# Performance work log

Hardware: AMD Instinct MI355X
Metric: run time of the kernel (lower is better)

## Reference

```python
import jax, jax.numpy as jnp
import numpy as np

B, L, E, H = 2, 2048, 512, 8
D = E // H  # head_dim = 64


def setup_inputs() -> dict:
    key = jax.random.key(0)
    ks = jax.random.split(key, 12)
    s = 0.02
    return {
        "values": jax.random.normal(ks[0], (B, L, E), jnp.float32),
        "keys": jax.random.normal(ks[1], (B, L, E), jnp.float32),
        "query": jax.random.normal(ks[2], (B, L, E), jnp.float32),
        "mask": jax.random.randint(ks[3], (B, 1, L, L), 0, 2, jnp.int32),
        "Wv": jax.random.normal(ks[4], (E, E), jnp.float32) * s,
        "bv": jax.random.normal(ks[5], (E,), jnp.float32) * s,
        "Wk": jax.random.normal(ks[6], (E, E), jnp.float32) * s,
        "bk": jax.random.normal(ks[7], (E,), jnp.float32) * s,
        "Wq": jax.random.normal(ks[8], (E, E), jnp.float32) * s,
        "bq": jax.random.normal(ks[9], (E,), jnp.float32) * s,
        "Wo": jax.random.normal(ks[10], (E, E), jnp.float32) * s,
        "bo": jax.random.normal(ks[11], (E,), jnp.float32) * s,
    }


def reference(values, keys, query, mask, Wv, bv, Wk, bk, Wq, bq, Wo, bo):
    b, lq = query.shape[0], query.shape[1]
    # torch Linear: y = x @ W.T + b
    v = (values @ Wv.T + bv).reshape(b, -1, H, D)
    k = (keys @ Wk.T + bk).reshape(b, -1, H, D)
    q = (query @ Wq.T + bq).reshape(b, lq, H, D)
    energy = jnp.einsum("bqhd,bkhd->bhqk", q, k)  # [B,H,Lq,Lk]
    # mask applied BEFORE the scale, as in the original
    energy = jnp.where(mask == 0, jnp.float32(-1e20), energy)
    # NOTE: scales by sqrt(embed_size), not sqrt(head_dim) (faithful)
    attn = jax.nn.softmax(energy / jnp.sqrt(jnp.float32(E)), axis=3)
    out = jnp.einsum("bhql,blhd->bqhd", attn, v).reshape(b, lq, E)
    return out @ Wo.T + bo
```

## Files before the change

### kernel.cpp

```cpp
#include <hip/hip_runtime.h>
#include <hip/hip_bf16.h>
#include <math.h>

#define BB 2
#define LL 2048
#define EE 512
#define HH 8
#define DD 64
#define MM (BB * LL)
#define LW (LL / 64)
#define NSP 2
#define NT (LW / NSP)

typedef short bf16x8 __attribute__((ext_vector_type(8)));
typedef float f32x4 __attribute__((ext_vector_type(4)));
typedef float f32x16 __attribute__((ext_vector_type(16)));

#define MFMA16(a, b, c) __builtin_amdgcn_mfma_f32_16x16x32_bf16((a), (b), (c), 0, 0, 0)
#define MFMA32(a, b, c) __builtin_amdgcn_mfma_f32_32x32x16_bf16((a), (b), (c), 0, 0, 0)

#if __has_builtin(__builtin_amdgcn_exp2f)
#define EXP2(x) __builtin_amdgcn_exp2f(x)
#else
#define EXP2(x) exp2f(x)
#endif

#define QSCALE 0.0637587146f

__device__ __forceinline__ void gl2lds16(const __hip_bfloat16* g, __hip_bfloat16* l) {
    __builtin_amdgcn_global_load_lds(
        (const __attribute__((address_space(1))) unsigned int*)(g),
        (__attribute__((address_space(3))) unsigned int*)(l),
        16, 0, 0);
}

__device__ __forceinline__ uint4 cvt8_bf16(const float4 a, const float4 b) {
    union { __hip_bfloat16 h[8]; uint4 u; } t;
    t.h[0] = __float2bfloat16(a.x); t.h[1] = __float2bfloat16(a.y);
    t.h[2] = __float2bfloat16(a.z); t.h[3] = __float2bfloat16(a.w);
    t.h[4] = __float2bfloat16(b.x); t.h[5] = __float2bfloat16(b.y);
    t.h[6] = __float2bfloat16(b.z); t.h[7] = __float2bfloat16(b.w);
    return t.u;
}

struct PrepArgs {
    const float* xsrc[3];
    __hip_bfloat16* xdst[3];
    const float* wsrc[4];
    __hip_bfloat16* wdst[4];
    const int* mask;
    unsigned long long* mbits;
};

__global__ __launch_bounds__(256) void prep(PrepArgs a) {
    const int blk = blockIdx.x;
    if (blk < 3072) {
        const int t = blk >> 10;
        const int i = ((blk & 1023) * 256 + threadIdx.x) * 8;
        const float* s = a.xsrc[t] + i;
        float4 f0 = *(const float4*)(s);
        float4 f1 = *(const float4*)(s + 4);
        *(uint4*)(a.xdst[t] + i) = cvt8_bf16(f0, f1);
    } else if (blk < 3584) {
        const int r = blk - 3072;
        const int t = r >> 7;
        const int i = ((r & 127) * 256 + threadIdx.x) * 8;
        const float* s = a.wsrc[t] + i;
        float4 f0 = *(const float4*)(s);
        float4 f1 = *(const float4*)(s + 4);
        *(uint4*)(a.wdst[t] + i) = cvt8_bf16(f0, f1);
    } else {
        const int mb = blk - 3584;
        #pragma unroll
        for (int r = 0; r < 16; ++r) {
            const size_t idx = ((size_t)mb * 16 + r) * 256 + threadIdx.x;
            const int m = a.mask[idx];
            const unsigned long long w = __ballot(m != 0);
            if ((threadIdx.x & 63) == 0) a.mbits[idx >> 6] = w;
        }
    }
}

struct QKVArgs {
    const __hip_bfloat16* X[3];
    const __hip_bfloat16* W[3];
    const float* bias[3];
    __hip_bfloat16* O[3];
};

__global__ __launch_bounds__(256) void gemm_qkv(QKVArgs p) {
    __shared__ __hip_bfloat16 As[2][2][64][32];
    __shared__ __hip_bfloat16 Bs[2][2][128][32];

    const int z = blockIdx.z;
    const __hip_bfloat16* __restrict__ X = p.X[z];
    const __hip_bfloat16* __restrict__ W = p.W[z];
    const float* __restrict__ bias = p.bias[z];
    __hip_bfloat16* __restrict__ O = p.O[z];

    const int tid = threadIdx.x;
    const int wave = tid >> 6, lane = tid & 63;
    const int l15 = lane & 15, quad = lane >> 4;
    const int wn = wave * 32;
    const int m0 = blockIdx.y * 64, n0 = blockIdx.x * 128;

    const int lr = lane >> 2;
    const int lc = (lane & 3) * 8;
    const __hip_bfloat16* Ax = X + (size_t)(m0 + wave * 16 + lr) * EE + lc;
    const __hip_bfloat16* Bx = W + (size_t)(n0 + wave * 32 + lr) * EE + lc;

    f32x4 acc[4][2] = {};

    #define STAGE_G(buf, k0)                                                   \
        gl2lds16(Ax + (k0),           &As[buf][0][wave * 16][0]);              \
        gl2lds16(Ax + (k0) + 32,      &As[buf][1][wave * 16][0]);              \
        gl2lds16(Bx + (k0),           &Bs[buf][0][wave * 32][0]);              \
        gl2lds16(Bx + (k0) + 32,      &Bs[buf][1][wave * 32][0]);              \
        gl2lds16(Bx + (k0) + 16 * EE,      &Bs[buf][0][wave * 32 + 16][0]);    \
        gl2lds16(Bx + (k0) + 16 * EE + 32, &Bs[buf][1][wave * 32 + 16][0]);

    STAGE_G(0, 0);
    __syncthreads();

    for (int kt = 0; kt < 8; ++kt) {
        const int cur = kt & 1;
        if (kt < 7) { STAGE_G(cur ^ 1, (kt + 1) * 64); }

        #pragma unroll
        for (int c = 0; c < 2; ++c) {
            bf16x8 af[4], bf2[2];
            #pragma unroll
            for (int i = 0; i < 4; ++i)
                af[i] = *(const bf16x8*)&As[cur][c][i * 16 + l15][quad * 8];
            #pragma unroll
            for (int j = 0; j < 2; ++j)
                bf2[j] = *(const bf16x8*)&Bs[cur][c][wn + j * 16 + l15][quad * 8];
            #pragma unroll
            for (int i = 0; i < 4; ++i)
                #pragma unroll
                for (int j = 0; j < 2; ++j)
                    acc[i][j] = MFMA16(af[i], bf2[j], acc[i][j]);
        }
        __syncthreads();
    }

    if (z == 2) {
        #pragma unroll
        for (int i = 0; i < 4; ++i)
            #pragma unroll
            for (int j = 0; j < 2; ++j) {
                const int n = n0 + wn + j * 16 + l15;
                const float bv = bias[n];
                const int h = n >> 6, d = n & 63;
                union { __hip_bfloat16 hh[4]; ushort4 v4; } pk;
                #pragma unroll
                for (int reg = 0; reg < 4; ++reg)
                    pk.hh[reg] = __float2bfloat16(acc[i][j][reg] + bv);
                const int m = m0 + i * 16 + quad * 4;
                const int bb = m >> 11, l = m & 2047;
                *(ushort4*)&O[(((size_t)bb * HH + h) * DD + d) * LL + l] = pk.v4;
            }
    } else {
        const float oscale = (z == 0) ? QSCALE : 1.0f;
        #pragma unroll
        for (int i = 0; i < 4; ++i)
            #pragma unroll
            for (int j = 0; j < 2; ++j) {
                const int n = n0 + wn + j * 16 + l15;
                const float bv = bias[n];
                #pragma unroll
                for (int reg = 0; reg < 4; ++reg) {
                    const int m = m0 + i * 16 + quad * 4 + reg;
                    O[(size_t)m * EE + n] = __float2bfloat16((acc[i][j][reg] + bv) * oscale);
                }
            }
    }
}

__global__ __launch_bounds__(256) void gemm_out(
    const __hip_bfloat16* __restrict__ X, const __hip_bfloat16* __restrict__ W,
    const float* __restrict__ bias, float* __restrict__ C) {
    __shared__ __hip_bfloat16 As[2][2][64][32];
    __shared__ __hip_bfloat16 Bs[2][2][128][32];

    const int tid = threadIdx.x;
    const int wave = tid >> 6, lane = tid & 63;
    const int l15 = lane & 15, quad = lane >> 4;
    const int wn = wave * 32;
    const int m0 = blockIdx.y * 64, n0 = blockIdx.x * 128;

    const int lr = lane >> 2;
    const int lc = (lane & 3) * 8;
    const __hip_bfloat16* Ax = X + (size_t)(m0 + wave * 16 + lr) * EE + lc;
    const __hip_bfloat16* Bx = W + (size_t)(n0 + wave * 32 + lr) * EE + lc;

    f32x4 acc[4][2] = {};

    STAGE_G(0, 0);
    __syncthreads();

    for (int kt = 0; kt < 8; ++kt) {
        const int cur = kt & 1;
        if (kt < 7) { STAGE_G(cur ^ 1, (kt + 1) * 64); }

        #pragma unroll
        for (int c = 0; c < 2; ++c) {
            bf16x8 af[4], bf2[2];
            #pragma unroll
            for (int i = 0; i < 4; ++i)
                af[i] = *(const bf16x8*)&As[cur][c][i * 16 + l15][quad * 8];
            #pragma unroll
            for (int j = 0; j < 2; ++j)
                bf2[j] = *(const bf16x8*)&Bs[cur][c][wn + j * 16 + l15][quad * 8];
            #pragma unroll
            for (int i = 0; i < 4; ++i)
                #pragma unroll
                for (int j = 0; j < 2; ++j)
                    acc[i][j] = MFMA16(af[i], bf2[j], acc[i][j]);
        }
        __syncthreads();
    }

    #pragma unroll
    for (int i = 0; i < 4; ++i)
        #pragma unroll
        for (int j = 0; j < 2; ++j) {
            const int n = n0 + wn + j * 16 + l15;
            const float bv = bias[n];
            #pragma unroll
            for (int reg = 0; reg < 4; ++reg) {
                const int m = m0 + i * 16 + quad * 4 + reg;
                C[(size_t)m * EE + n] = acc[i][j][reg] + bv;
            }
        }
}

__global__ __launch_bounds__(256, 2) void attn_mfma(
    const __hip_bfloat16* __restrict__ Qb, const __hip_bfloat16* __restrict__ Kb,
    const __hip_bfloat16* __restrict__ vtg, const unsigned long long* __restrict__ mbits,
    float* __restrict__ Op, float* __restrict__ lp) {
    __shared__ __hip_bfloat16 Ks[2][64][68];
    __shared__ __hip_bfloat16 Vs[2][64][68];

    const int tid = threadIdx.x;
    const int wave = tid >> 6, lane = tid & 63;
    const int l31 = lane & 31, hi = lane >> 5;

    const int flat = blockIdx.x;
    const int c = flat & 7;
    const int i = flat >> 3;
    const int gl = i >> 4;
    const int qx = i & 15;
    const int g = c * 4 + gl;
    const int sp = g & 1;
    const int rem = g >> 1;
    const int h = rem & 7;
    const int b = rem >> 3;
    const int q0 = qx * 128;
    const int qrow = q0 + wave * 32 + l31;

    const int srow = tid >> 2, sc0 = (tid & 3) * 16;
    const int t0 = sp * NT;

    bf16x8 qf[4];
    {
        const __hip_bfloat16* qr = Qb + ((size_t)b * LL + qrow) * EE + h * DD + hi * 8;
        qf[0] = *(const bf16x8*)(qr);
        qf[1] = *(const bf16x8*)(qr + 16);
        qf[2] = *(const bf16x8*)(qr + 32);
        qf[3] = *(const bf16x8*)(qr + 48);
    }

    const __hip_bfloat16* kbase =
        Kb + ((size_t)b * LL + (size_t)t0 * 64 + srow) * EE + h * DD + sc0;
    const __hip_bfloat16* vbase =
        vtg + (((size_t)b * HH + h) * DD + srow) * LL + (size_t)t0 * 64 + sc0;
    const unsigned long long* mrow = mbits + ((size_t)b * LL + qrow) * LW + t0;

    f32x16 o0 = {}, o1 = {};
    float lrun = 0.f;

    {
        uint4 k0 = *(const uint4*)(kbase);
        uint4 k1 = *(const uint4*)(kbase + 8);
        uint4 v0 = *(const uint4*)(vbase);
        uint4 v1 = *(const uint4*)(vbase + 8);
        *(uint4*)&Ks[0][srow][sc0] = k0;
        *(uint4*)&Ks[0][srow][sc0 + 8] = k1;
        *(uint4*)&Vs[0][srow][sc0] = v0;
        *(uint4*)&Vs[0][srow][sc0 + 8] = v1;
    }
    unsigned long long mw_cur = mrow[0];
    __syncthreads();

    for (int t = 0; t < NT; ++t) {
        const int cur = t & 1, nxt = cur ^ 1;
        const bool more = (t + 1) < NT;

        uint4 kn0, kn1, vn0, vn1;
        unsigned long long mw_n;
        if (more) {
            const __hip_bfloat16* kp = kbase + (size_t)(t + 1) * 64 * EE;
            const __hip_bfloat16* vp = vbase + (t + 1) * 64;
            kn0 = *(const uint4*)(kp);
            kn1 = *(const uint4*)(kp + 8);
            vn0 = *(const uint4*)(vp);
            vn1 = *(const uint4*)(vp + 8);
            mw_n = mrow[t + 1];
        }

        f32x16 st0 = {}, st1 = {};
        __builtin_amdgcn_s_setprio(1);
        #pragma unroll
        for (int kk = 0; kk < 4; ++kk) {
            bf16x8 kf0 = *(const bf16x8*)&Ks[cur][l31][kk * 16 + hi * 8];
            bf16x8 kf1 = *(const bf16x8*)&Ks[cur][32 + l31][kk * 16 + hi * 8];
            st0 = MFMA32(kf0, qf[kk], st0);
            st1 = MFMA32(kf1, qf[kk], st1);
        }
        __builtin_amdgcn_s_setprio(0);

        const unsigned long long msh = mw_cur >> (4 * hi);
        const unsigned int m32a = (unsigned int)msh;
        const unsigned int m32b = (unsigned int)(msh >> 32);
        bf16x8 pa[4];
        #pragma unroll
        for (int kt = 0; kt < 2; ++kt) {
            const f32x16 stv = kt ? st1 : st0;
            const unsigned int mm = kt ? m32b : m32a;
            float p[16];
            #pragma unroll
            for (int r = 0; r < 16; ++r) {
                const int bit = (r & 3) + 8 * (r >> 2);
                const float e = EXP2(stv[r]);
                p[r] = ((mm >> bit) & 1u) ? e : 0.f;
            }
            lrun += (((p[0] + p[1]) + (p[2] + p[3])) + ((p[4] + p[5]) + (p[6] + p[7])))
                  + (((p[8] + p[9]) + (p[10] + p[11])) + ((p[12] + p[13]) + (p[14] + p[15])));
            unsigned int w[8];
            #pragma unroll
            for (int i2 = 0; i2 < 8; ++i2) {
                union { __hip_bfloat162 h2; unsigned int u; } cv;
                cv.h2 = __float22bfloat162_rn(make_float2(p[2 * i2], p[2 * i2 + 1]));
                w[i2] = cv.u;
            }
            asm volatile("v_permlane32_swap_b32 %0, %1" : "+v"(w[0]), "+v"(w[2]));
            asm volatile("v_permlane32_swap_b32 %0, %1" : "+v"(w[1]), "+v"(w[3]));
            asm volatile("v_permlane32_swap_b32 %0, %1" : "+v"(w[4]), "+v"(w[6]));
            asm volatile("v_permlane32_swap_b32 %0, %1" : "+v"(w[5]), "+v"(w[7]));
            union { unsigned int u[4]; bf16x8 v; } f0, f1;
            f0.u[0] = w[0]; f0.u[1] = w[1]; f0.u[2] = w[2]; f0.u[3] = w[3];
            f1.u[0] = w[4]; f1.u[1] = w[5]; f1.u[2] = w[6]; f1.u[3] = w[7];
            pa[kt * 2] = f0.v;
            pa[kt * 2 + 1] = f1.v;
        }

        __builtin_amdgcn_s_setprio(1);
        #pragma unroll
        for (int wd = 0; wd < 4; ++wd) {
            bf16x8 vf0 = *(const bf16x8*)&Vs[cur][l31][wd * 16 + hi * 8];
            bf16x8 vf1 = *(const bf16x8*)&Vs[cur][32 + l31][wd * 16 + hi * 8];
            o0 = MFMA32(pa[wd], vf0, o0);
            o1 = MFMA32(pa[wd], vf1, o1);
        }
        __builtin_amdgcn_s_setprio(0);

        if (more) {
            *(uint4*)&Ks[nxt][srow][sc0] = kn0;
            *(uint4*)&Ks[nxt][srow][sc0 + 8] = kn1;
            *(uint4*)&Vs[nxt][srow][sc0] = vn0;
            *(uint4*)&Vs[nxt][srow][sc0 + 8] = vn1;
            mw_cur = mw_n;
        }
        __syncthreads();
    }

    lrun += __shfl_xor(lrun, 32);
    if (hi == 0)
        lp[(((size_t)sp * BB + b) * HH + h) * LL + qrow] = lrun;

    float* Ob = Op + (size_t)sp * MM * EE
              + ((size_t)b * LL + q0 + wave * 32) * EE + h * DD;
    #pragma unroll
    for (int r = 0; r < 16; ++r) {
        const int qr = (r & 3) + 8 * (r >> 2) + 4 * hi;
        Ob[(size_t)qr * EE + l31] = o0[r];
        Ob[(size_t)qr * EE + 32 + l31] = o1[r];
    }
}

__global__ __launch_bounds__(256) void combine(
    const float* __restrict__ Op, const float* __restrict__ lp,
    __hip_bfloat16* __restrict__ aob) {
    const int idx = blockIdx.x * 256 + threadIdx.x;
    const int row = idx >> 6;
    const int c0 = (idx & 63) * 8;
    const int b = row >> 11, q = row & 2047;
    const int h = c0 >> 6;
    float lsum = 0.f;
    float4 s0 = make_float4(0.f, 0.f, 0.f, 0.f);
    float4 s1 = make_float4(0.f, 0.f, 0.f, 0.f);
    #pragma unroll
    for (int sp = 0; sp < NSP; ++sp) {
        lsum += lp[(((size_t)sp * BB + b) * HH + h) * LL + q];
        const float* p = Op + (size_t)sp * MM * EE + (size_t)row * EE + c0;
        float4 a0 = *(const float4*)(p);
        float4 a1 = *(const float4*)(p + 4);
        s0.x += a0.x; s0.y += a0.y; s0.z += a0.z; s0.w += a0.w;
        s1.x += a1.x; s1.y += a1.y; s1.z += a1.z; s1.w += a1.w;
    }
    const float linv = 1.f / lsum;
    union { __hip_bfloat16 hh[8]; uint4 u; } pk;
    pk.hh[0] = __float2bfloat16(s0.x * linv);
    pk.hh[1] = __float2bfloat16(s0.y * linv);
    pk.hh[2] = __float2bfloat16(s0.z * linv);
    pk.hh[3] = __float2bfloat16(s0.w * linv);
    pk.hh[4] = __float2bfloat16(s1.x * linv);
    pk.hh[5] = __float2bfloat16(s1.y * linv);
    pk.hh[6] = __float2bfloat16(s1.z * linv);
    pk.hh[7] = __float2bfloat16(s1.w * linv);
    *(uint4*)&aob[(size_t)row * EE + c0] = pk.u;
}

extern "C" void kernel_launch(void* const* d_in, const int* in_sizes, int n_in,
                              void* d_out, int out_size, void* d_ws, size_t ws_size,
                              hipStream_t stream) {
    const float* values = (const float*)d_in[0];
    const float* keys   = (const float*)d_in[1];
    const float* query  = (const float*)d_in[2];
    const int*   mask   = (const int*)d_in[3];
    const float* Wv = (const float*)d_in[4];
    const float* bv = (const float*)d_in[5];
    const float* Wk = (const float*)d_in[6];
    const float* bk = (const float*)d_in[7];
    const float* Wq = (const float*)d_in[8];
    const float* bq = (const float*)d_in[9];
    const float* Wo = (const float*)d_in[10];
    const float* bo = (const float*)d_in[11];
    float* out = (float*)d_out;

    const size_t XS = (size_t)MM * EE * 2;
    const size_t WS = (size_t)EE * EE * 2;
    const size_t MBSZ = (size_t)BB * LL * LL / 8;
    const size_t OPSZ = (size_t)MM * EE * 4;
    char* w = (char*)d_ws;
    __hip_bfloat16* xq  = (__hip_bfloat16*)(w);
    __hip_bfloat16* xk  = (__hip_bfloat16*)(w + XS);
    __hip_bfloat16* xv  = (__hip_bfloat16*)(w + 2 * XS);
    __hip_bfloat16* qb  = (__hip_bfloat16*)(w + 3 * XS);
    __hip_bfloat16* kb  = (__hip_bfloat16*)(w + 4 * XS);
    __hip_bfloat16* vtg = (__hip_bfloat16*)(w + 5 * XS);
    __hip_bfloat16* aob = (__hip_bfloat16*)(w + 6 * XS);
    __hip_bfloat16* wqb = (__hip_bfloat16*)(w + 7 * XS);
    __hip_bfloat16* wkb = (__hip_bfloat16*)(w + 7 * XS + WS);
    __hip_bfloat16* wvb = (__hip_bfloat16*)(w + 7 * XS + 2 * WS);
    __hip_bfloat16* wob = (__hip_bfloat16*)(w + 7 * XS + 3 * WS);
    unsigned long long* mbits = (unsigned long long*)(w + 7 * XS + 4 * WS);
    float* Op = (float*)(w + 7 * XS + 4 * WS + MBSZ);
    float* lp = (float*)(w + 7 * XS + 4 * WS + MBSZ + NSP * OPSZ);

    PrepArgs pa;
    pa.xsrc[0] = query; pa.xsrc[1] = keys; pa.xsrc[2] = values;
    pa.xdst[0] = xq;    pa.xdst[1] = xk;   pa.xdst[2] = xv;
    pa.wsrc[0] = Wq; pa.wsrc[1] = Wk; pa.wsrc[2] = Wv; pa.wsrc[3] = Wo;
    pa.wdst[0] = wqb; pa.wdst[1] = wkb; pa.wdst[2] = wvb; pa.wdst[3] = wob;
    pa.mask = mask; pa.mbits = mbits;

    QKVArgs qa;
    qa.X[0] = xq;  qa.X[1] = xk;  qa.X[2] = xv;
    qa.W[0] = wqb; qa.W[1] = wkb; qa.W[2] = wvb;
    qa.bias[0] = bq; qa.bias[1] = bk; qa.bias[2] = bv;
    qa.O[0] = qb;  qa.O[1] = kb;  qa.O[2] = vtg;

    prep<<<5632, 256, 0, stream>>>(pa);
    gemm_qkv<<<dim3(EE / 128, MM / 64, 3), 256, 0, stream>>>(qa);
    attn_mfma<<<dim3(512, 1, 1), 256, 0, stream>>>(qb, kb, vtg, mbits, Op, lp);
    combine<<<(MM * EE) / 2048, 256, 0, stream>>>(Op, lp, aob);
    gemm_out<<<dim3(EE / 128, MM / 64), 256, 0, stream>>>(aob, wob, bo, out);
}
```

Measured before the change: 179.7 us.

## Enlarge GEMM tiles to 128x128 and give attention waves 64 query rows

The QKV and output GEMMs now use 128x128 block tiles, with each wave computing a 64x64 sub-tile. This doubles the MFMA work per LDS fragment load and halves the grid. The attention kernel drops to 2 waves of 128 threads, each handling two 32-row query groups, so every K/V LDS fragment feeds twice as many MFMAs. The V prefetch load is also moved after the softmax. In exchange it raises register pressure, lowers the number of waves per block, and reduces grid parallelism.

```diff
diff --git a/kernel.cpp b/kernel.cpp
--- a/kernel.cpp
+++ b/kernel.cpp
@@ -89,7 +89,7 @@
 };
 
 __global__ __launch_bounds__(256) void gemm_qkv(QKVArgs p) {
-    __shared__ __hip_bfloat16 As[2][2][64][32];
+    __shared__ __hip_bfloat16 As[2][2][128][32];
     __shared__ __hip_bfloat16 Bs[2][2][128][32];
 
     const int z = blockIdx.z;
@@ -101,22 +101,24 @@
     const int tid = threadIdx.x;
     const int wave = tid >> 6, lane = tid & 63;
     const int l15 = lane & 15, quad = lane >> 4;
-    const int wn = wave * 32;
-    const int m0 = blockIdx.y * 64, n0 = blockIdx.x * 128;
+    const int wr = (wave >> 1) * 64, wc = (wave & 1) * 64;
+    const int m0 = blockIdx.y * 128, n0 = blockIdx.x * 128;
 
     const int lr = lane >> 2;
     const int lc = (lane & 3) * 8;
-    const __hip_bfloat16* Ax = X + (size_t)(m0 + wave * 16 + lr) * EE + lc;
+    const __hip_bfloat16* Ax = X + (size_t)(m0 + wave * 32 + lr) * EE + lc;
     const __hip_bfloat16* Bx = W + (size_t)(n0 + wave * 32 + lr) * EE + lc;
 
-    f32x4 acc[4][2] = {};
-
-    #define STAGE_G(buf, k0)                                                   \
-        gl2lds16(Ax + (k0),           &As[buf][0][wave * 16][0]);              \
-        gl2lds16(Ax + (k0) + 32,      &As[buf][1][wave * 16][0]);              \
-        gl2lds16(Bx + (k0),           &Bs[buf][0][wave * 32][0]);              \
-        gl2lds16(Bx + (k0) + 32,      &Bs[buf][1][wave * 32][0]);              \
-        gl2lds16(Bx + (k0) + 16 * EE,      &Bs[buf][0][wave * 32 + 16][0]);    \
+    f32x4 acc[4][4] = {};
+
+    #define STAGE_G(buf, k0)                                                       \
+        gl2lds16(Ax + (k0),                &As[buf][0][wave * 32][0]);             \
+        gl2lds16(Ax + (k0) + 16 * EE,      &As[buf][0][wave * 32 + 16][0]);        \
+        gl2lds16(Ax + (k0) + 32,           &As[buf][1][wave * 32][0]);             \
+        gl2lds16(Ax + (k0) + 16 * EE + 32, &As[buf][1][wave * 32 + 16][0]);        \
+        gl2lds16(Bx + (k0),                &Bs[buf][0][wave * 32][0]);             \
+        gl2lds16(Bx + (k0) + 16 * EE,      &Bs[buf][0][wave * 32 + 16][0]);        \
+        gl2lds16(Bx + (k0) + 32,           &Bs[buf][1][wave * 32][0]);             \
         gl2lds16(Bx + (k0) + 16 * EE + 32, &Bs[buf][1][wave * 32 + 16][0]);
 
     STAGE_G(0, 0);
@@ -128,18 +130,18 @@
 
         #pragma unroll
         for (int c = 0; c < 2; ++c) {
-            bf16x8 af[4], bf2[2];
+            bf16x8 af[4], bf[4];
             #pragma unroll
             for (int i = 0; i < 4; ++i)
-                af[i] = *(const bf16x8*)&As[cur][c][i * 16 + l15][quad * 8];
-            #pragma unroll
-            for (int j = 0; j < 2; ++j)
-                bf2[j] = *(const bf16x8*)&Bs[cur][c][wn + j * 16 + l15][quad * 8];
+                af[i] = *(const bf16x8*)&As[cur][c][wr + i * 16 + l15][quad * 8];
+            #pragma unroll
+            for (int j = 0; j < 4; ++j)
+                bf[j] = *(const bf16x8*)&Bs[cur][c][wc + j * 16 + l15][quad * 8];
             #pragma unroll
             for (int i = 0; i < 4; ++i)
                 #pragma unroll
-                for (int j = 0; j < 2; ++j)
-                    acc[i][j] = MFMA16(af[i], bf2[j], acc[i][j]);
+                for (int j = 0; j < 4; ++j)
+                    acc[i][j] = MFMA16(af[i], bf[j], acc[i][j]);
         }
         __syncthreads();
     }
@@ -148,15 +150,15 @@
         #pragma unroll
         for (int i = 0; i < 4; ++i)
             #pragma unroll
-            for (int j = 0; j < 2; ++j) {
-                const int n = n0 + wn + j * 16 + l15;
+            for (int j = 0; j < 4; ++j) {
+                const int n = n0 + wc + j * 16 + l15;
                 const float bv = bias[n];
                 const int h = n >> 6, d = n & 63;
                 union { __hip_bfloat16 hh[4]; ushort4 v4; } pk;
                 #pragma unroll
                 for (int reg = 0; reg < 4; ++reg)
                     pk.hh[reg] = __float2bfloat16(acc[i][j][reg] + bv);
-                const int m = m0 + i * 16 + quad * 4;
+                const int m = m0 + wr + i * 16 + quad * 4;
                 const int bb = m >> 11, l = m & 2047;
                 *(ushort4*)&O[(((size_t)bb * HH + h) * DD + d) * LL + l] = pk.v4;
             }
@@ -165,12 +167,12 @@
         #pragma unroll
         for (int i = 0; i < 4; ++i)
             #pragma unroll
-            for (int j = 0; j < 2; ++j) {
-                const int n = n0 + wn + j * 16 + l15;
+            for (int j = 0; j < 4; ++j) {
+                const int n = n0 + wc + j * 16 + l15;
                 const float bv = bias[n];
                 #pragma unroll
                 for (int reg = 0; reg < 4; ++reg) {
-                    const int m = m0 + i * 16 + quad * 4 + reg;
+                    const int m = m0 + wr + i * 16 + quad * 4 + reg;
                     O[(size_t)m * EE + n] = __float2bfloat16((acc[i][j][reg] + bv) * oscale);
                 }
             }
@@ -180,21 +182,21 @@
 __global__ __launch_bounds__(256) void gemm_out(
     const __hip_bfloat16* __restrict__ X, const __hip_bfloat16* __restrict__ W,
     const float* __restrict__ bias, float* __restrict__ C) {
-    __shared__ __hip_bfloat16 As[2][2][64][32];
+    __shared__ __hip_bfloat16 As[2][2][128][32];
     __shared__ __hip_bfloat16 Bs[2][2][128][32];
 
     const int tid = threadIdx.x;
     const int wave = tid >> 6, lane = tid & 63;
     const int l15 = lane & 15, quad = lane >> 4;
-    const int wn = wave * 32;
-    const int m0 = blockIdx.y * 64, n0 = blockIdx.x * 128;
+    const int wr = (wave >> 1) * 64, wc = (wave & 1) * 64;
+    const int m0 = blockIdx.y * 128, n0 = blockIdx.x * 128;
 
     const int lr = lane >> 2;
     const int lc = (lane & 3) * 8;
-    const __hip_bfloat16* Ax = X + (size_t)(m0 + wave * 16 + lr) * EE + lc;
+    const __hip_bfloat16* Ax = X + (size_t)(m0 + wave * 32 + lr) * EE + lc;
     const __hip_bfloat16* Bx = W + (size_t)(n0 + wave * 32 + lr) * EE + lc;
 
-    f32x4 acc[4][2] = {};
+    f32x4 acc[4][4] = {};
 
     STAGE_G(0, 0);
     __syncthreads();
@@ -205,18 +207,18 @@
 
         #pragma unroll
         for (int c = 0; c < 2; ++c) {
-            bf16x8 af[4], bf2[2];
+            bf16x8 af[4], bf[4];
             #pragma unroll
             for (int i = 0; i < 4; ++i)
-                af[i] = *(const bf16x8*)&As[cur][c][i * 16 + l15][quad * 8];
-            #pragma unroll
-            for (int j = 0; j < 2; ++j)
-                bf2[j] = *(const bf16x8*)&Bs[cur][c][wn + j * 16 + l15][quad * 8];
+                af[i] = *(const bf16x8*)&As[cur][c][wr + i * 16 + l15][quad * 8];
+            #pragma unroll
+            for (int j = 0; j < 4; ++j)
+                bf[j] = *(const bf16x8*)&Bs[cur][c][wc + j * 16 + l15][quad * 8];
             #pragma unroll
             for (int i = 0; i < 4; ++i)
                 #pragma unroll
-                for (int j = 0; j < 2; ++j)
-                    acc[i][j] = MFMA16(af[i], bf2[j], acc[i][j]);
+                for (int j = 0; j < 4; ++j)
+                    acc[i][j] = MFMA16(af[i], bf[j], acc[i][j]);
         }
         __syncthreads();
     }
@@ -224,18 +226,18 @@
     #pragma unroll
     for (int i = 0; i < 4; ++i)
         #pragma unroll
-        for (int j = 0; j < 2; ++j) {
-            const int n = n0 + wn + j * 16 + l15;
+        for (int j = 0; j < 4; ++j) {
+            const int n = n0 + wc + j * 16 + l15;
             const float bv = bias[n];
             #pragma unroll
             for (int reg = 0; reg < 4; ++reg) {
-                const int m = m0 + i * 16 + quad * 4 + reg;
+                const int m = m0 + wr + i * 16 + quad * 4 + reg;
                 C[(size_t)m * EE + n] = acc[i][j][reg] + bv;
             }
         }
 }
 
-__global__ __launch_bounds__(256, 2) void attn_mfma(
+__global__ __launch_bounds__(128, 2) void attn_mfma(
     const __hip_bfloat16* __restrict__ Qb, const __hip_bfloat16* __restrict__ Kb,
     const __hip_bfloat16* __restrict__ vtg, const unsigned long long* __restrict__ mbits,
     float* __restrict__ Op, float* __restrict__ lp) {
@@ -257,102 +259,131 @@
     const int h = rem & 7;
     const int b = rem >> 3;
     const int q0 = qx * 128;
-    const int qrow = q0 + wave * 32 + l31;
-
-    const int srow = tid >> 2, sc0 = (tid & 3) * 16;
+    const int qrow0 = q0 + wave * 64 + l31;
+    const int qrow1 = qrow0 + 32;
+
+    const int srow = tid >> 1, sc0 = (tid & 1) * 32;
     const int t0 = sp * NT;
 
-    bf16x8 qf[4];
+    bf16x8 qf0[4], qf1[4];
     {
-        const __hip_bfloat16* qr = Qb + ((size_t)b * LL + qrow) * EE + h * DD + hi * 8;
-        qf[0] = *(const bf16x8*)(qr);
-        qf[1] = *(const bf16x8*)(qr + 16);
-        qf[2] = *(const bf16x8*)(qr + 32);
-        qf[3] = *(const bf16x8*)(qr + 48);
+        const __hip_bfloat16* qr0 = Qb + ((size_t)b * LL + qrow0) * EE + h * DD + hi * 8;
+        const __hip_bfloat16* qr1 = Qb + ((size_t)b * LL + qrow1) * EE + h * DD + hi * 8;
+        #pragma unroll
+        for (int kk = 0; kk < 4; ++kk) {
+            qf0[kk] = *(const bf16x8*)(qr0 + kk * 16);
+            qf1[kk] = *(const bf16x8*)(qr1 + kk * 16);
+        }
     }
 
     const __hip_bfloat16* kbase =
         Kb + ((size_t)b * LL + (size_t)t0 * 64 + srow) * EE + h * DD + sc0;
     const __hip_bfloat16* vbase =
         vtg + (((size_t)b * HH + h) * DD + srow) * LL + (size_t)t0 * 64 + sc0;
-    const unsigned long long* mrow = mbits + ((size_t)b * LL + qrow) * LW + t0;
-
-    f32x16 o0 = {}, o1 = {};
-    float lrun = 0.f;
+    const unsigned long long* mrow0 = mbits + ((size_t)b * LL + qrow0) * LW + t0;
+    const unsigned long long* mrow1 = mbits + ((size_t)b * LL + qrow1) * LW + t0;
+
+    f32x16 o00 = {}, o01 = {}, o10 = {}, o11 = {};
+    float lrun0 = 0.f, lrun1 = 0.f;
 
     {
         uint4 k0 = *(const uint4*)(kbase);
         uint4 k1 = *(const uint4*)(kbase + 8);
+        uint4 k2 = *(const uint4*)(kbase + 16);
+        uint4 k3 = *(const uint4*)(kbase + 24);
         uint4 v0 = *(const uint4*)(vbase);
         uint4 v1 = *(const uint4*)(vbase + 8);
+        uint4 v2 = *(const uint4*)(vbase + 16);
+        uint4 v3 = *(const uint4*)(vbase + 24);
         *(uint4*)&Ks[0][srow][sc0] = k0;
         *(uint4*)&Ks[0][srow][sc0 + 8] = k1;
+        *(uint4*)&Ks[0][srow][sc0 + 16] = k2;
+        *(uint4*)&Ks[0][srow][sc0 + 24] = k3;
         *(uint4*)&Vs[0][srow][sc0] = v0;
         *(uint4*)&Vs[0][srow][sc0 + 8] = v1;
-    }
-    unsigned long long mw_cur = mrow[0];
+        *(uint4*)&Vs[0][srow][sc0 + 16] = v2;
+        *(uint4*)&Vs[0][srow][sc0 + 24] = v3;
+    }
+    unsigned long long mw0 = mrow0[0], mw1 = mrow1[0];
     __syncthreads();
+
+    #define SMAX(S0, S1, MW, LR, PA)                                               \
+    {                                                                              \
+        const unsigned long long msh = (MW) >> (4 * hi);                           \
+        const unsigned int m32a = (unsigned int)msh;                               \
+        const unsigned int m32b = (unsigned int)(msh >> 32);                       \
+        _Pragma("unroll")                                                          \
+        for (int kt = 0; kt < 2; ++kt) {                                           \
+            const f32x16 stv = kt ? (S1) : (S0);                                   \
+            const unsigned int mm = kt ? m32b : m32a;                              \
+            float p[16];                                                           \
+            _Pragma("unroll")                                                      \
+            for (int r = 0; r < 16; ++r) {                                         \
+                const int bit = (r & 3) + 8 * (r >> 2);                            \
+                const float e = EXP2(stv[r]);                                      \
+                p[r] = ((mm >> bit) & 1u) ? e : 0.f;                               \
+            }                                                                      \
+            (LR) += (((p[0]+p[1])+(p[2]+p[3]))+((p[4]+p[5])+(p[6]+p[7])))          \
+                  + (((p[8]+p[9])+(p[10]+p[11]))+((p[12]+p[13])+(p[14]+p[15])));   \
+            unsigned int w[8];                                                     \
+            _Pragma("unroll")                                                      \
+            for (int i2 = 0; i2 < 8; ++i2) {                                       \
+                union { __hip_bfloat162 h2; unsigned int u; } cv;                  \
+                cv.h2 = __float22bfloat162_rn(make_float2(p[2*i2], p[2*i2+1]));    \
+                w[i2] = cv.u;                                                      \
+            }                                                                      \
+            asm volatile("v_permlane32_swap_b32 %0, %1" : "+v"(w[0]), "+v"(w[2])); \
+            asm volatile("v_permlane32_swap_b32 %0, %1" : "+v"(w[1]), "+v"(w[3])); \
+            asm volatile("v_permlane32_swap_b32 %0, %1" : "+v"(w[4]), "+v"(w[6])); \
+            asm volatile("v_permlane32_swap_b32 %0, %1" : "+v"(w[5]), "+v"(w[7])); \
+            union { unsigned int u[4]; bf16x8 v; } f0, f1;                         \
+            f0.u[0] = w[0]; f0.u[1] = w[1]; f0.u[2] = w[2]; f0.u[3] = w[3];        \
+            f1.u[0] = w[4]; f1.u[1] = w[5]; f1.u[2] = w[6]; f1.u[3] = w[7];        \
+            (PA)[kt * 2] = f0.v;                                                   \
+            (PA)[kt * 2 + 1] = f1.v;                                               \
+        }                                                                          \
+    }
 
     for (int t = 0; t < NT; ++t) {
         const int cur = t & 1, nxt = cur ^ 1;
         const bool more = (t + 1) < NT;
 
-        uint4 kn0, kn1, vn0, vn1;
-        unsigned long long mw_n;
+        uint4 kn0, kn1, kn2, kn3;
+        unsigned long long mwn0, mwn1;
         if (more) {
             const __hip_bfloat16* kp = kbase + (size_t)(t + 1) * 64 * EE;
-            const __hip_bfloat16* vp = vbase + (t + 1) * 64;
             kn0 = *(const uint4*)(kp);
             kn1 = *(const uint4*)(kp + 8);
-            vn0 = *(const uint4*)(vp);
-            vn1 = *(const uint4*)(vp + 8);
-            mw_n = mrow[t + 1];
-        }
-
-        f32x16 st0 = {}, st1 = {};
+            kn2 = *(const uint4*)(kp + 16);
+            kn3 = *(const uint4*)(kp + 24);
+            mwn0 = mrow0[t + 1];
+            mwn1 = mrow1[t + 1];
+        }
+
+        f32x16 s00 = {}, s01 = {}, s10 = {}, s11 = {};
         __builtin_amdgcn_s_setprio(1);
         #pragma unroll
         for (int kk = 0; kk < 4; ++kk) {
             bf16x8 kf0 = *(const bf16x8*)&Ks[cur][l31][kk * 16 + hi * 8];
             bf16x8 kf1 = *(const bf16x8*)&Ks[cur][32 + l31][kk * 16 + hi * 8];
-            st0 = MFMA32(kf0, qf[kk], st0);
-            st1 = MFMA32(kf1, qf[kk], st1);
+            s00 = MFMA32(kf0, qf0[kk], s00);
+            s01 = MFMA32(kf1, qf0[kk], s01);
+            s10 = MFMA32(kf0, qf1[kk], s10);
+            s11 = MFMA32(kf1, qf1[kk], s11);
         }
         __builtin_amdgcn_s_setprio(0);
 
-        const unsigned long long msh = mw_cur >> (4 * hi);
-        const unsigned int m32a = (unsigned int)msh;
-        const unsigned int m32b = (unsigned int)(msh >> 32);
-        bf16x8 pa[4];
-        #pragma unroll
-        for (int kt = 0; kt < 2; ++kt) {
-            const f32x16 stv = kt ? st1 : st0;
-            const unsigned int mm = kt ? m32b : m32a;
-            float p[16];
-            #pragma unroll
-            for (int r = 0; r < 16; ++r) {
-                const int bit = (r & 3) + 8 * (r >> 2);
-                const float e = EXP2(stv[r]);
-                p[r] = ((mm >> bit) & 1u) ? e : 0.f;
-            }
-            lrun += (((p[0] + p[1]) + (p[2] + p[3])) + ((p[4] + p[5]) + (p[6] + p[7])))
-                  + (((p[8] + p[9]) + (p[10] + p[11])) + ((p[12] + p[13]) + (p[14] + p[15])));
-            unsigned int w[8];
-            #pragma unroll
-            for (int i2 = 0; i2 < 8; ++i2) {
-                union { __hip_bfloat162 h2; unsigned int u; } cv;
-                cv.h2 = __float22bfloat162_rn(make_float2(p[2 * i2], p[2 * i2 + 1]));
-                w[i2] = cv.u;
-            }
-            asm volatile("v_permlane32_swap_b32 %0, %1" : "+v"(w[0]), "+v"(w[2]));
-            asm volatile("v_permlane32_swap_b32 %0, %1" : "+v"(w[1]), "+v"(w[3]));
-            asm volatile("v_permlane32_swap_b32 %0, %1" : "+v"(w[4]), "+v"(w[6]));
-            asm volatile("v_permlane32_swap_b32 %0, %1" : "+v"(w[5]), "+v"(w[7]));
-            union { unsigned int u[4]; bf16x8 v; } f0, f1;
-            f0.u[0] = w[0]; f0.u[1] = w[1]; f0.u[2] = w[2]; f0.u[3] = w[3];
-            f1.u[0] = w[4]; f1.u[1] = w[5]; f1.u[2] = w[6]; f1.u[3] = w[7];
-            pa[kt * 2] = f0.v;
-            pa[kt * 2 + 1] = f1.v;
+        bf16x8 pa0[4], pa1[4];
+        SMAX(s00, s01, mw0, lrun0, pa0);
+        SMAX(s10, s11, mw1, lrun1, pa1);
+
+        uint4 vn0, vn1, vn2, vn3;
+        if (more) {
+            const __hip_bfloat16* vp = vbase + (t + 1) * 64;
+            vn0 = *(const uint4*)(vp);
+            vn1 = *(const uint4*)(vp + 8);
+            vn2 = *(const uint4*)(vp + 16);
+            vn3 = *(const uint4*)(vp + 24);
         }
 
         __builtin_amdgcn_s_setprio(1);
@@ -360,32 +391,45 @@
         for (int wd = 0; wd < 4; ++wd) {
             bf16x8 vf0 = *(const bf16x8*)&Vs[cur][l31][wd * 16 + hi * 8];
             bf16x8 vf1 = *(const bf16x8*)&Vs[cur][32 + l31][wd * 16 + hi * 8];
-            o0 = MFMA32(pa[wd], vf0, o0);
-            o1 = MFMA32(pa[wd], vf1, o1);
+            o00 = MFMA32(pa0[wd], vf0, o00);
+            o01 = MFMA32(pa0[wd], vf1, o01);
+            o10 = MFMA32(pa1[wd], vf0, o10);
+            o11 = MFMA32(pa1[wd], vf1, o11);
         }
         __builtin_amdgcn_s_setprio(0);
 
         if (more) {
             *(uint4*)&Ks[nxt][srow][sc0] = kn0;
             *(uint4*)&Ks[nxt][srow][sc0 + 8] = kn1;
+            *(uint4*)&Ks[nxt][srow][sc0 + 16] = kn2;
+            *(uint4*)&Ks[nxt][srow][sc0 + 24] = kn3;
             *(uint4*)&Vs[nxt][srow][sc0] = vn0;
             *(uint4*)&Vs[nxt][srow][sc0 + 8] = vn1;
-            mw_cur = mw_n;
+            *(uint4*)&Vs[nxt][srow][sc0 + 16] = vn2;
+            *(uint4*)&Vs[nxt][srow][sc0 + 24] = vn3;
+            mw0 = mwn0;
+            mw1 = mwn1;
         }
         __syncthreads();
     }
 
-    lrun += __shfl_xor(lrun, 32);
-    if (hi == 0)
-        lp[(((size_t)sp * BB + b) * HH + h) * LL + qrow] = lrun;
-
-    float* Ob = Op + (size_t)sp * MM * EE
-              + ((size_t)b * LL + q0 + wave * 32) * EE + h * DD;
+    lrun0 += __shfl_xor(lrun0, 32);
+    lrun1 += __shfl_xor(lrun1, 32);
+    if (hi == 0) {
+        lp[(((size_t)sp * BB + b) * HH + h) * LL + qrow0] = lrun0;
+        lp[(((size_t)sp * BB + b) * HH + h) * LL + qrow1] = lrun1;
+    }
+
+    float* Ob0 = Op + (size_t)sp * MM * EE
+               + ((size_t)b * LL + q0 + wave * 64) * EE + h * DD;
+    float* Ob1 = Ob0 + (size_t)32 * EE;
     #pragma unroll
     for (int r = 0; r < 16; ++r) {
         const int qr = (r & 3) + 8 * (r >> 2) + 4 * hi;
-        Ob[(size_t)qr * EE + l31] = o0[r];
-        Ob[(size_t)qr * EE + 32 + l31] = o1[r];
+        Ob0[(size_t)qr * EE + l31] = o00[r];
+        Ob0[(size_t)qr * EE + 32 + l31] = o01[r];
+        Ob1[(size_t)qr * EE + l31] = o10[r];
+        Ob1[(size_t)qr * EE + 32 + l31] = o11[r];
     }
 }
 
@@ -473,8 +517,8 @@
     qa.O[0] = qb;  qa.O[1] = kb;  qa.O[2] = vtg;
 
     prep<<<5632, 256, 0, stream>>>(pa);
-    gemm_qkv<<<dim3(EE / 128, MM / 64, 3), 256, 0, stream>>>(qa);
-    attn_mfma<<<dim3(512, 1, 1), 256, 0, stream>>>(qb, kb, vtg, mbits, Op, lp);
+    gemm_qkv<<<dim3(EE / 128, MM / 128, 3), 256, 0, stream>>>(qa);
+    attn_mfma<<<dim3(512, 1, 1), 128, 0, stream>>>(qb, kb, vtg, mbits, Op, lp);
     combine<<<(MM * EE) / 2048, 256, 0, stream>>>(Op, lp, aob);
-    gemm_out<<<dim3(EE / 128, MM / 64), 256, 0, stream>>>(aob, wob, bo, out);
-}
+    gemm_out<<<dim3(EE / 128, MM / 128), 256, 0, stream>>>(aob, wob, bo, out);
+}
```

New measurement: 200.7 us. 1.12x slower.

## Enlarge GEMM tiles to 128x128 with 2x2 wave layout and XCD-aware block mapping

Applied to the files above, without the earlier changes.

Both projection GEMMs move from 64x128 tiles with waves split along N to 128x128 tiles with a 2x2 wave grid, so each wave computes 64x64 and reuses each A/B fragment four times. The 3D grid becomes a flat 1D grid whose index is remapped so that consecutive blocks on the same XCD share A rows, which improves L2 reuse. The cost is half as many blocks (384 and 128 on a many-CU GPU), which lowers occupancy and wave-level parallelism, plus more accumulator registers.

```diff
diff --git a/kernel.cpp b/kernel.cpp
--- a/kernel.cpp
+++ b/kernel.cpp
@@ -89,10 +89,17 @@
 };
 
 __global__ __launch_bounds__(256) void gemm_qkv(QKVArgs p) {
-    __shared__ __hip_bfloat16 As[2][2][64][32];
+    __shared__ __hip_bfloat16 As[2][2][128][32];
     __shared__ __hip_bfloat16 Bs[2][2][128][32];
 
-    const int z = blockIdx.z;
+    const int flat = blockIdx.x;
+    const int cx = flat & 7;
+    const int s = flat >> 3;
+    const int xn = s & 3;
+    const int g = cx * 12 + (s >> 2);
+    const int z = g >> 5;
+    const int ym = g & 31;
+
     const __hip_bfloat16* __restrict__ X = p.X[z];
     const __hip_bfloat16* __restrict__ W = p.W[z];
     const float* __restrict__ bias = p.bias[z];
@@ -101,22 +108,24 @@
     const int tid = threadIdx.x;
     const int wave = tid >> 6, lane = tid & 63;
     const int l15 = lane & 15, quad = lane >> 4;
-    const int wn = wave * 32;
-    const int m0 = blockIdx.y * 64, n0 = blockIdx.x * 128;
+    const int wr = (wave >> 1) * 64, wc = (wave & 1) * 64;
+    const int m0 = ym * 128, n0 = xn * 128;
 
     const int lr = lane >> 2;
     const int lc = (lane & 3) * 8;
-    const __hip_bfloat16* Ax = X + (size_t)(m0 + wave * 16 + lr) * EE + lc;
+    const __hip_bfloat16* Ax = X + (size_t)(m0 + wave * 32 + lr) * EE + lc;
     const __hip_bfloat16* Bx = W + (size_t)(n0 + wave * 32 + lr) * EE + lc;
 
-    f32x4 acc[4][2] = {};
-
-    #define STAGE_G(buf, k0)                                                   \
-        gl2lds16(Ax + (k0),           &As[buf][0][wave * 16][0]);              \
-        gl2lds16(Ax + (k0) + 32,      &As[buf][1][wave * 16][0]);              \
-        gl2lds16(Bx + (k0),           &Bs[buf][0][wave * 32][0]);              \
-        gl2lds16(Bx + (k0) + 32,      &Bs[buf][1][wave * 32][0]);              \
-        gl2lds16(Bx + (k0) + 16 * EE,      &Bs[buf][0][wave * 32 + 16][0]);    \
+    f32x4 acc[4][4] = {};
+
+    #define STAGE_G(buf, k0)                                                       \
+        gl2lds16(Ax + (k0),                &As[buf][0][wave * 32][0]);             \
+        gl2lds16(Ax + (k0) + 16 * EE,      &As[buf][0][wave * 32 + 16][0]);        \
+        gl2lds16(Ax + (k0) + 32,           &As[buf][1][wave * 32][0]);             \
+        gl2lds16(Ax + (k0) + 16 * EE + 32, &As[buf][1][wave * 32 + 16][0]);        \
+        gl2lds16(Bx + (k0),                &Bs[buf][0][wave * 32][0]);             \
+        gl2lds16(Bx + (k0) + 16 * EE,      &Bs[buf][0][wave * 32 + 16][0]);        \
+        gl2lds16(Bx + (k0) + 32,           &Bs[buf][1][wave * 32][0]);             \
         gl2lds16(Bx + (k0) + 16 * EE + 32, &Bs[buf][1][wave * 32 + 16][0]);
 
     STAGE_G(0, 0);
@@ -128,18 +137,18 @@
 
         #pragma unroll
         for (int c = 0; c < 2; ++c) {
-            bf16x8 af[4], bf2[2];
+            bf16x8 af[4], bf[4];
             #pragma unroll
             for (int i = 0; i < 4; ++i)
-                af[i] = *(const bf16x8*)&As[cur][c][i * 16 + l15][quad * 8];
-            #pragma unroll
-            for (int j = 0; j < 2; ++j)
-                bf2[j] = *(const bf16x8*)&Bs[cur][c][wn + j * 16 + l15][quad * 8];
+                af[i] = *(const bf16x8*)&As[cur][c][wr + i * 16 + l15][quad * 8];
+            #pragma unroll
+            for (int j = 0; j < 4; ++j)
+                bf[j] = *(const bf16x8*)&Bs[cur][c][wc + j * 16 + l15][quad * 8];
             #pragma unroll
             for (int i = 0; i < 4; ++i)
                 #pragma unroll
-                for (int j = 0; j < 2; ++j)
-                    acc[i][j] = MFMA16(af[i], bf2[j], acc[i][j]);
+                for (int j = 0; j < 4; ++j)
+                    acc[i][j] = MFMA16(af[i], bf[j], acc[i][j]);
         }
         __syncthreads();
     }
@@ -148,15 +157,15 @@
         #pragma unroll
         for (int i = 0; i < 4; ++i)
             #pragma unroll
-            for (int j = 0; j < 2; ++j) {
-                const int n = n0 + wn + j * 16 + l15;
+            for (int j = 0; j < 4; ++j) {
+                const int n = n0 + wc + j * 16 + l15;
                 const float bv = bias[n];
                 const int h = n >> 6, d = n & 63;
                 union { __hip_bfloat16 hh[4]; ushort4 v4; } pk;
                 #pragma unroll
                 for (int reg = 0; reg < 4; ++reg)
                     pk.hh[reg] = __float2bfloat16(acc[i][j][reg] + bv);
-                const int m = m0 + i * 16 + quad * 4;
+                const int m = m0 + wr + i * 16 + quad * 4;
                 const int bb = m >> 11, l = m & 2047;
                 *(ushort4*)&O[(((size_t)bb * HH + h) * DD + d) * LL + l] = pk.v4;
             }
@@ -165,12 +174,12 @@
         #pragma unroll
         for (int i = 0; i < 4; ++i)
             #pragma unroll
-            for (int j = 0; j < 2; ++j) {
-                const int n = n0 + wn + j * 16 + l15;
+            for (int j = 0; j < 4; ++j) {
+                const int n = n0 + wc + j * 16 + l15;
                 const float bv = bias[n];
                 #pragma unroll
                 for (int reg = 0; reg < 4; ++reg) {
-                    const int m = m0 + i * 16 + quad * 4 + reg;
+                    const int m = m0 + wr + i * 16 + quad * 4 + reg;
                     O[(size_t)m * EE + n] = __float2bfloat16((acc[i][j][reg] + bv) * oscale);
                 }
             }
@@ -180,21 +189,27 @@
 __global__ __launch_bounds__(256) void gemm_out(
     const __hip_bfloat16* __restrict__ X, const __hip_bfloat16* __restrict__ W,
     const float* __restrict__ bias, float* __restrict__ C) {
-    __shared__ __hip_bfloat16 As[2][2][64][32];
+    __shared__ __hip_bfloat16 As[2][2][128][32];
     __shared__ __hip_bfloat16 Bs[2][2][128][32];
+
+    const int flat = blockIdx.x;
+    const int cx = flat & 7;
+    const int s = flat >> 3;
+    const int xn = s & 3;
+    const int ym = cx * 4 + (s >> 2);
 
     const int tid = threadIdx.x;
     const int wave = tid >> 6, lane = tid & 63;
     const int l15 = lane & 15, quad = lane >> 4;
-    const int wn = wave * 32;
-    const int m0 = blockIdx.y * 64, n0 = blockIdx.x * 128;
+    const int wr = (wave >> 1) * 64, wc = (wave & 1) * 64;
+    const int m0 = ym * 128, n0 = xn * 128;
 
     const int lr = lane >> 2;
     const int lc = (lane & 3) * 8;
-    const __hip_bfloat16* Ax = X + (size_t)(m0 + wave * 16 + lr) * EE + lc;
+    const __hip_bfloat16* Ax = X + (size_t)(m0 + wave * 32 + lr) * EE + lc;
     const __hip_bfloat16* Bx = W + (size_t)(n0 + wave * 32 + lr) * EE + lc;
 
-    f32x4 acc[4][2] = {};
+    f32x4 acc[4][4] = {};
 
     STAGE_G(0, 0);
     __syncthreads();
@@ -205,18 +220,18 @@
 
         #pragma unroll
         for (int c = 0; c < 2; ++c) {
-            bf16x8 af[4], bf2[2];
+            bf16x8 af[4], bf[4];
             #pragma unroll
             for (int i = 0; i < 4; ++i)
-                af[i] = *(const bf16x8*)&As[cur][c][i * 16 + l15][quad * 8];
-            #pragma unroll
-            for (int j = 0; j < 2; ++j)
-                bf2[j] = *(const bf16x8*)&Bs[cur][c][wn + j * 16 + l15][quad * 8];
+                af[i] = *(const bf16x8*)&As[cur][c][wr + i * 16 + l15][quad * 8];
+            #pragma unroll
+            for (int j = 0; j < 4; ++j)
+                bf[j] = *(const bf16x8*)&Bs[cur][c][wc + j * 16 + l15][quad * 8];
             #pragma unroll
             for (int i = 0; i < 4; ++i)
                 #pragma unroll
-                for (int j = 0; j < 2; ++j)
-                    acc[i][j] = MFMA16(af[i], bf2[j], acc[i][j]);
+                for (int j = 0; j < 4; ++j)
+                    acc[i][j] = MFMA16(af[i], bf[j], acc[i][j]);
         }
         __syncthreads();
     }
@@ -224,12 +239,12 @@
     #pragma unroll
     for (int i = 0; i < 4; ++i)
         #pragma unroll
-        for (int j = 0; j < 2; ++j) {
-            const int n = n0 + wn + j * 16 + l15;
+        for (int j = 0; j < 4; ++j) {
+            const int n = n0 + wc + j * 16 + l15;
             const float bv = bias[n];
             #pragma unroll
             for (int reg = 0; reg < 4; ++reg) {
-                const int m = m0 + i * 16 + quad * 4 + reg;
+                const int m = m0 + wr + i * 16 + quad * 4 + reg;
                 C[(size_t)m * EE + n] = acc[i][j][reg] + bv;
             }
         }
@@ -473,8 +488,8 @@
     qa.O[0] = qb;  qa.O[1] = kb;  qa.O[2] = vtg;
 
     prep<<<5632, 256, 0, stream>>>(pa);
-    gemm_qkv<<<dim3(EE / 128, MM / 64, 3), 256, 0, stream>>>(qa);
+    gemm_qkv<<<dim3(384, 1, 1), 256, 0, stream>>>(qa);
     attn_mfma<<<dim3(512, 1, 1), 256, 0, stream>>>(qb, kb, vtg, mbits, Op, lp);
     combine<<<(MM * EE) / 2048, 256, 0, stream>>>(Op, lp, aob);
-    gemm_out<<<dim3(EE / 128, MM / 64), 256, 0, stream>>>(aob, wob, bo, out);
-}
+    gemm_out<<<dim3(128, 1, 1), 256, 0, stream>>>(aob, wob, bo, out);
+}
```

Result: slower. 183.8 us (+2.3%).

## Fuse split-K combine into output projection GEMM A-tile loading

Applied to the files above, without the earlier changes.

Removes the separate combine kernel. The output GEMM now reads the two fp32 partial attention outputs and row sums directly, normalizes them, converts to bf16 in registers and writes its own A tiles to LDS, while the weight tiles still use the direct global-to-LDS copy. This drops one launch and the bf16 intermediate round trip. In exchange each A row is read once per column block, four times in total, as fp32, with register-staged prefetch. The grid is also flattened with a swizzled block order, so blocks sharing M rows run close together for cache reuse.

```diff
diff --git a/kernel.cpp b/kernel.cpp
--- a/kernel.cpp
+++ b/kernel.cpp
@@ -178,30 +178,80 @@
 }
 
 __global__ __launch_bounds__(256) void gemm_out(
-    const __hip_bfloat16* __restrict__ X, const __hip_bfloat16* __restrict__ W,
-    const float* __restrict__ bias, float* __restrict__ C) {
+    const float* __restrict__ Op, const float* __restrict__ lp,
+    const __hip_bfloat16* __restrict__ W, const float* __restrict__ bias,
+    float* __restrict__ C) {
     __shared__ __hip_bfloat16 As[2][2][64][32];
     __shared__ __hip_bfloat16 Bs[2][2][128][32];
+
+    const int flat = blockIdx.x;
+    const int cx = flat & 7;
+    const int s = flat >> 3;
+    const int xn = s & 3;
+    const int ym = cx * 8 + (s >> 2);
 
     const int tid = threadIdx.x;
     const int wave = tid >> 6, lane = tid & 63;
     const int l15 = lane & 15, quad = lane >> 4;
     const int wn = wave * 32;
-    const int m0 = blockIdx.y * 64, n0 = blockIdx.x * 128;
+    const int m0 = ym * 64, n0 = xn * 128;
 
     const int lr = lane >> 2;
     const int lc = (lane & 3) * 8;
-    const __hip_bfloat16* Ax = X + (size_t)(m0 + wave * 16 + lr) * EE + lc;
+    const int mrow = m0 + wave * 16 + lr;
+    const int bb = mrow >> 11, qq = mrow & 2047;
+    const float* Ax0 = Op + (size_t)mrow * EE + lc;
+    const float* Ax1 = Ax0 + (size_t)MM * EE;
+    const float* lq0 = lp + (size_t)bb * HH * LL + qq;
+    const float* lq1 = lp + ((size_t)(BB + bb)) * HH * LL + qq;
     const __hip_bfloat16* Bx = W + (size_t)(n0 + wave * 32 + lr) * EE + lc;
 
     f32x4 acc[4][2] = {};
 
-    STAGE_G(0, 0);
+    float4 ar[8];
+    float lsum;
+
+    #define LOAD_A(k0)                                                         \
+        lsum = lq0[(size_t)((k0) >> 6) * LL] + lq1[(size_t)((k0) >> 6) * LL];  \
+        ar[0] = *(const float4*)(Ax0 + (k0));                                  \
+        ar[1] = *(const float4*)(Ax0 + (k0) + 4);                              \
+        ar[2] = *(const float4*)(Ax0 + (k0) + 32);                             \
+        ar[3] = *(const float4*)(Ax0 + (k0) + 36);                             \
+        ar[4] = *(const float4*)(Ax1 + (k0));                                  \
+        ar[5] = *(const float4*)(Ax1 + (k0) + 4);                              \
+        ar[6] = *(const float4*)(Ax1 + (k0) + 32);                             \
+        ar[7] = *(const float4*)(Ax1 + (k0) + 36);
+
+    #define WRITE_A(buf)                                                       \
+        {                                                                      \
+            const float linv = 1.f / lsum;                                     \
+            float4 s0, s1;                                                     \
+            s0.x = (ar[0].x + ar[4].x) * linv; s0.y = (ar[0].y + ar[4].y) * linv; \
+            s0.z = (ar[0].z + ar[4].z) * linv; s0.w = (ar[0].w + ar[4].w) * linv; \
+            s1.x = (ar[1].x + ar[5].x) * linv; s1.y = (ar[1].y + ar[5].y) * linv; \
+            s1.z = (ar[1].z + ar[5].z) * linv; s1.w = (ar[1].w + ar[5].w) * linv; \
+            *(uint4*)&As[buf][0][wave * 16 + lr][lc] = cvt8_bf16(s0, s1);      \
+            s0.x = (ar[2].x + ar[6].x) * linv; s0.y = (ar[2].y + ar[6].y) * linv; \
+            s0.z = (ar[2].z + ar[6].z) * linv; s0.w = (ar[2].w + ar[6].w) * linv; \
+            s1.x = (ar[3].x + ar[7].x) * linv; s1.y = (ar[3].y + ar[7].y) * linv; \
+            s1.z = (ar[3].z + ar[7].z) * linv; s1.w = (ar[3].w + ar[7].w) * linv; \
+            *(uint4*)&As[buf][1][wave * 16 + lr][lc] = cvt8_bf16(s0, s1);      \
+        }
+
+    #define STAGE_B(buf, k0)                                                   \
+        gl2lds16(Bx + (k0),                &Bs[buf][0][wave * 32][0]);         \
+        gl2lds16(Bx + (k0) + 32,           &Bs[buf][1][wave * 32][0]);         \
+        gl2lds16(Bx + (k0) + 16 * EE,      &Bs[buf][0][wave * 32 + 16][0]);    \
+        gl2lds16(Bx + (k0) + 16 * EE + 32, &Bs[buf][1][wave * 32 + 16][0]);
+
+    LOAD_A(0);
+    STAGE_B(0, 0);
+    WRITE_A(0);
     __syncthreads();
 
     for (int kt = 0; kt < 8; ++kt) {
         const int cur = kt & 1;
-        if (kt < 7) { STAGE_G(cur ^ 1, (kt + 1) * 64); }
+        if (kt < 7) { LOAD_A((kt + 1) * 64); STAGE_B(cur ^ 1, (kt + 1) * 64); }
 
         #pragma unroll
         for (int c = 0; c < 2; ++c) {
@@ -218,6 +268,7 @@
                 for (int j = 0; j < 2; ++j)
                     acc[i][j] = MFMA16(af[i], bf2[j], acc[i][j]);
         }
+        if (kt < 7) { WRITE_A(cur ^ 1); }
         __syncthreads();
     }
 
@@ -387,39 +438,6 @@
         Ob[(size_t)qr * EE + l31] = o0[r];
         Ob[(size_t)qr * EE + 32 + l31] = o1[r];
     }
-}
-
-__global__ __launch_bounds__(256) void combine(
-    const float* __restrict__ Op, const float* __restrict__ lp,
-    __hip_bfloat16* __restrict__ aob) {
-    const int idx = blockIdx.x * 256 + threadIdx.x;
-    const int row = idx >> 6;
-    const int c0 = (idx & 63) * 8;
-    const int b = row >> 11, q = row & 2047;
-    const int h = c0 >> 6;
-    float lsum = 0.f;
-    float4 s0 = make_float4(0.f, 0.f, 0.f, 0.f);
-    float4 s1 = make_float4(0.f, 0.f, 0.f, 0.f);
-    #pragma unroll
-    for (int sp = 0; sp < NSP; ++sp) {
-        lsum += lp[(((size_t)sp * BB + b) * HH + h) * LL + q];
-        const float* p = Op + (size_t)sp * MM * EE + (size_t)row * EE + c0;
-        float4 a0 = *(const float4*)(p);
-        float4 a1 = *(const float4*)(p + 4);
-        s0.x += a0.x; s0.y += a0.y; s0.z += a0.z; s0.w += a0.w;
-        s1.x += a1.x; s1.y += a1.y; s1.z += a1.z; s1.w += a1.w;
-    }
-    const float linv = 1.f / lsum;
-    union { __hip_bfloat16 hh[8]; uint4 u; } pk;
-    pk.hh[0] = __float2bfloat16(s0.x * linv);
-    pk.hh[1] = __float2bfloat16(s0.y * linv);
-    pk.hh[2] = __float2bfloat16(s0.z * linv);
-    pk.hh[3] = __float2bfloat16(s0.w * linv);
-    pk.hh[4] = __float2bfloat16(s1.x * linv);
-    pk.hh[5] = __float2bfloat16(s1.y * linv);
-    pk.hh[6] = __float2bfloat16(s1.z * linv);
-    pk.hh[7] = __float2bfloat16(s1.w * linv);
-    *(uint4*)&aob[(size_t)row * EE + c0] = pk.u;
 }
 
 extern "C" void kernel_launch(void* const* d_in, const int* in_sizes, int n_in,
@@ -450,7 +468,6 @@
     __hip_bfloat16* qb  = (__hip_bfloat16*)(w + 3 * XS);
     __hip_bfloat16* kb  = (__hip_bfloat16*)(w + 4 * XS);
     __hip_bfloat16* vtg = (__hip_bfloat16*)(w + 5 * XS);
-    __hip_bfloat16* aob = (__hip_bfloat16*)(w + 6 * XS);
     __hip_bfloat16* wqb = (__hip_bfloat16*)(w + 7 * XS);
     __hip_bfloat16* wkb = (__hip_bfloat16*)(w + 7 * XS + WS);
     __hip_bfloat16* wvb = (__hip_bfloat16*)(w + 7 * XS + 2 * WS);
@@ -475,6 +492,5 @@
     prep<<<5632, 256, 0, stream>>>(pa);
     gemm_qkv<<<dim3(EE / 128, MM / 64, 3), 256, 0, stream>>>(qa);
     attn_mfma<<<dim3(512, 1, 1), 256, 0, stream>>>(qb, kb, vtg, mbits, Op, lp);
-    combine<<<(MM * EE) / 2048, 256, 0, stream>>>(Op, lp, aob);
-    gemm_out<<<dim3(EE / 128, MM / 64), 256, 0, stream>>>(aob, wob, bo, out);
-}
+    gemm_out<<<dim3(256, 1, 1), 256, 0, stream>>>(Op, lp, wob, bo, out);
+}
```

Result: no change. 177.3 us, median of 2 (-1.4%).
